# Kernel optimization log

Measured on AMD Instinct MI355X. Metric: run time of the kernel, lower is better.

## Reference

```python
import jax, jax.numpy as jnp
import numpy as np

N_NODES = 100000
N_EDGES = 3200000
NEG_SLOPE = 0.2


def setup_inputs() -> dict:
    key = jax.random.key(0)
    k = jax.random.split(key, 7)
    feat = jax.random.normal(k[0], (N_NODES, 256), dtype=jnp.float32)
    W_fc = jax.random.normal(k[1], (64, 256), dtype=jnp.float32) * 0.05
    attn_l = jax.random.normal(k[2], (4, 16), dtype=jnp.float32) * 0.1
    attn_r = jax.random.normal(k[3], (4, 16), dtype=jnp.float32) * 0.1
    W_res = jax.random.normal(k[4], (64, 256), dtype=jnp.float32) * 0.05
    src = jax.random.randint(k[5], (N_EDGES,), 0, N_NODES, dtype=jnp.int32)
    dst = jax.random.randint(k[6], (N_EDGES,), 0, N_NODES, dtype=jnp.int32)
    return {"feat": feat, "W_fc": W_fc, "attn_l": attn_l, "attn_r": attn_r,
            "W_res": W_res, "src": src, "dst": dst}


def reference(feat, W_fc, attn_l, attn_r, W_res, src, dst):
    N = feat.shape[0]
    H, D = attn_l.shape
    # Linear projection -> per-head features [N, H, D]
    feat_src = (feat @ W_fc.T).reshape(N, H, D)
    # Per-node attention logits [N, H]
    el = jnp.einsum('nhd,hd->nh', feat_src, attn_l)
    er = jnp.einsum('nhd,hd->nh', feat_src, attn_r)
    # fused_gat: per-edge leaky-relu score, edge softmax over dst, scatter-sum
    e = jax.nn.leaky_relu(el[src] + er[dst], negative_slope=NEG_SLOPE)  # [E, H]
    emax = jax.ops.segment_max(e, dst, num_segments=N)  # [N, H]
    emax = jnp.where(jnp.isfinite(emax), emax, 0.0)  # zero-degree safety
    ee = jnp.exp(e - emax[dst])  # [E, H]
    denom = jax.ops.segment_sum(ee, dst, num_segments=N)  # [N, H]
    alpha = ee / jnp.maximum(denom[dst], 1e-20)  # [E, H]
    # weighted aggregation of source features -> [N, H, D]
    rst = jax.ops.segment_sum(alpha[:, :, None] * feat_src[src], dst,
                              num_segments=N)
    # residual connection (res_fc always present in this module)
    resval = (feat @ W_res.T).reshape(N, H, D)
    return rst + resval
```

## Files before the change

### kernel.cpp

```cpp
#include <hip/hip_runtime.h>
#include <hip/hip_bf16.h>


#define F_IN 256
#define O_OUT 64
#define NEG_SLOPE 0.2f
#define CHUNK 16384
#define RMAX 2048

using frag_ab = __attribute__((ext_vector_type(8))) short;
using frag_cd = __attribute__((ext_vector_type(4))) float;

__device__ __forceinline__ float lrelu(float x) {
    return x >= 0.0f ? x : NEG_SLOPE * x;
}

__device__ __forceinline__ unsigned short f2bf(float f) {
    unsigned int u = __float_as_uint(f);
    unsigned int r = (u + 0x7fffu + ((u >> 16) & 1u)) >> 16;
    return (unsigned short)r;
}
__device__ __forceinline__ float bflo(unsigned int p) {
    return __uint_as_float(p << 16);
}
__device__ __forceinline__ float bfhi(unsigned int p) {
    return __uint_as_float(p & 0xffff0000u);
}

__global__ __launch_bounds__(256) void wprep_kernel(
    const float* __restrict__ Wfc, const float* __restrict__ Wres,
    unsigned short* __restrict__ Bf)
{
    int tid = blockIdx.x * 256 + threadIdx.x;
    int ct = tid >> 9;
    int lane = tid & 63;
    int ks = (tid >> 6) & 7;
    int col = ct * 16 + (lane & 15);
    int kbase = ks * 32 + (lane >> 4) * 8;
    const float* srcW = (col < 64) ? (Wfc + (size_t)col * 256 + kbase)
                                   : (Wres + (size_t)(col - 64) * 256 + kbase);
    unsigned short* dstp = Bf + (size_t)tid * 8;
#pragma unroll
    for (int i = 0; i < 8; ++i) dstp[i] = f2bf(srcW[i]);
}

__global__ __launch_bounds__(256) void proj_mfma_kernel(
    const float* __restrict__ feat, const unsigned short* __restrict__ Bf,
    const float* __restrict__ attn_l, const float* __restrict__ attn_r,
    unsigned short* __restrict__ fsb, float* __restrict__ el,
    float* __restrict__ er, float* __restrict__ out,
    float* __restrict__ denom_zero, int N)
{
    __shared__ __align__(16) unsigned short sA[64 * 280];
    const int t = threadIdx.x;
    const int lane = t & 63;
    const int w = t >> 6;
    const int n0 = blockIdx.x * 64;
    if (n0 >= N) return;

    frag_ab bfrag[2][8];
    {
        const unsigned short* bp = Bf + (size_t)lane * 8;
#pragma unroll
        for (int j = 0; j < 2; ++j)
#pragma unroll
            for (int ks = 0; ks < 8; ++ks)
                bfrag[j][ks] = *(const frag_ab*)(bp + (size_t)((2 * w + j) * 8 + ks) * 512);
    }

    if (denom_zero && n0 * 4 + t < N * 4) denom_zero[n0 * 4 + t] = 0.0f;

    for (int i = 0; i < 8; ++i) {
        int f = i * 256 + t;
        int row = f >> 5, c8 = f & 31;
        int n = n0 + row;
        float4 v0 = make_float4(0.f, 0.f, 0.f, 0.f), v1 = v0;
        if (n < N) {
            const float4* p = (const float4*)(feat + (size_t)n * F_IN + c8 * 8);
            v0 = p[0]; v1 = p[1];
        }
        frag_ab pack;
        pack[0] = (short)f2bf(v0.x); pack[1] = (short)f2bf(v0.y);
        pack[2] = (short)f2bf(v0.z); pack[3] = (short)f2bf(v0.w);
        pack[4] = (short)f2bf(v1.x); pack[5] = (short)f2bf(v1.y);
        pack[6] = (short)f2bf(v1.z); pack[7] = (short)f2bf(v1.w);
        *(frag_ab*)(&sA[row * 280 + c8 * 8]) = pack;
    }
    __syncthreads();

    frag_cd acc[4][2];
#pragma unroll
    for (int rt = 0; rt < 4; ++rt)
#pragma unroll
        for (int j = 0; j < 2; ++j)
            acc[rt][j] = (frag_cd){0.f, 0.f, 0.f, 0.f};

#pragma unroll
    for (int ks = 0; ks < 8; ++ks) {
        frag_ab af[4];
#pragma unroll
        for (int rt = 0; rt < 4; ++rt) {
            int row = rt * 16 + (lane & 15);
            int c8 = ks * 4 + (lane >> 4);
            af[rt] = *(const frag_ab*)(&sA[row * 280 + c8 * 8]);
        }
#pragma unroll
        for (int rt = 0; rt < 4; ++rt)
#pragma unroll
            for (int j = 0; j < 2; ++j)
                acc[rt][j] = __builtin_amdgcn_mfma_f32_16x16x32_bf16(
                    af[rt], bfrag[j][ks], acc[rt][j], 0, 0, 0);
    }

    const int colq = lane & 15;
    const int quad = lane >> 4;
    if (w < 2) {
#pragma unroll
        for (int j = 0; j < 2; ++j) {
            int h = 2 * w + j;
            float al = attn_l[h * 16 + colq];
            float ar = attn_r[h * 16 + colq];
#pragma unroll
            for (int rt = 0; rt < 4; ++rt)
#pragma unroll
                for (int r = 0; r < 4; ++r) {
                    int node = n0 + rt * 16 + quad * 4 + r;
                    float v = acc[rt][j][r];
                    if (node < N) fsb[(size_t)node * O_OUT + h * 16 + colq] = f2bf(v);
                    float pl = v * al, pr = v * ar;
                    pl += __shfl_xor(pl, 1); pr += __shfl_xor(pr, 1);
                    pl += __shfl_xor(pl, 2); pr += __shfl_xor(pr, 2);
                    pl += __shfl_xor(pl, 4); pr += __shfl_xor(pr, 4);
                    pl += __shfl_xor(pl, 8); pr += __shfl_xor(pr, 8);
                    if (colq == 0 && node < N) {
                        el[(size_t)node * 4 + h] = pl;
                        er[(size_t)node * 4 + h] = pr;
                    }
                }
        }
    } else {
#pragma unroll
        for (int j = 0; j < 2; ++j) {
            int cb = 32 * (w - 2) + 16 * j;
#pragma unroll
            for (int rt = 0; rt < 4; ++rt)
#pragma unroll
                for (int r = 0; r < 4; ++r) {
                    int node = n0 + rt * 16 + quad * 4 + r;
                    if (node < N)
                        out[(size_t)node * O_OUT + cb + colq] = acc[rt][j][r];
                }
        }
    }
}

__global__ __launch_bounds__(256) void bucket_count_kernel(
    const int* __restrict__ dst, int* __restrict__ histT, int E, int B, int R)
{
    __shared__ int h[RMAX];
    int b = blockIdx.x, t = threadIdx.x;
    for (int i = t; i < R; i += 256) h[i] = 0;
    __syncthreads();
    int base = b * CHUNK;
    for (int i = t; i < CHUNK; i += 256) {
        int e = base + i;
        if (e < E) atomicAdd(&h[dst[e] >> 7], 1);
    }
    __syncthreads();
    for (int i = t; i < R; i += 256) histT[(size_t)i * B + b] = h[i];
}

__global__ __launch_bounds__(256) void scan_block_kernel(
    const int* __restrict__ counts, int* __restrict__ outp,
    int* __restrict__ bsums, int n)
{
    int t = threadIdx.x;
    int base = blockIdx.x * 1024 + t * 4;
    int c0 = 0, c1 = 0, c2 = 0, c3 = 0;
    if (base + 3 < n) {
        int4 v = *(const int4*)(counts + base);
        c0 = v.x; c1 = v.y; c2 = v.z; c3 = v.w;
    } else {
        if (base     < n) c0 = counts[base];
        if (base + 1 < n) c1 = counts[base + 1];
        if (base + 2 < n) c2 = counts[base + 2];
        if (base + 3 < n) c3 = counts[base + 3];
    }
    int tsum = c0 + c1 + c2 + c3;
    int inc = tsum;
    int lane = t & 63, wid = t >> 6;
#pragma unroll
    for (int o = 1; o < 64; o <<= 1) {
        int v = __shfl_up(inc, o);
        if (lane >= o) inc += v;
    }
    __shared__ int wsum[4];
    if (lane == 63) wsum[wid] = inc;
    __syncthreads();
    int woff = 0;
#pragma unroll
    for (int w = 0; w < 4; ++w)
        if (w < wid) woff += wsum[w];
    int excl = woff + inc - tsum;
    int e0 = excl, e1 = excl + c0, e2 = e1 + c1, e3 = e2 + c2;
    if (base + 3 < n) {
        *(int4*)(outp + base) = make_int4(e0, e1, e2, e3);
    } else {
        if (base     < n) outp[base]     = e0;
        if (base + 1 < n) outp[base + 1] = e1;
        if (base + 2 < n) outp[base + 2] = e2;
        if (base + 3 < n) outp[base + 3] = e3;
    }
    if (t == 255) bsums[blockIdx.x] = wsum[0] + wsum[1] + wsum[2] + wsum[3];
}

__global__ void scan_bsums_kernel(int* __restrict__ bsums, int nb)
{
    int lane = threadIdx.x;
    int carry = 0;
    for (int c = 0; c * 64 < nb; ++c) {
        int i = c * 64 + lane;
        int v = (i < nb) ? bsums[i] : 0;
        int inc = v;
#pragma unroll
        for (int o = 1; o < 64; o <<= 1) {
            int u = __shfl_up(inc, o);
            if (lane >= o) inc += u;
        }
        if (i < nb) bsums[i] = carry + inc - v;
        carry += __shfl(inc, 63);
    }
}

__global__ __launch_bounds__(256) void scan_final_kernel(
    int* __restrict__ outp, const int* __restrict__ bsums, int n, int total)
{
    int i = blockIdx.x * 256 + threadIdx.x;
    if (i < n) outp[i] = outp[i] + bsums[i >> 10];
    if (i == 0) outp[n] = total;
}

__global__ __launch_bounds__(256) void bucket_scatter_kernel(
    const int* __restrict__ src, const int* __restrict__ dst,
    const int* __restrict__ histS, unsigned int* __restrict__ sorted_pk,
    int E, int B, int R)
{
    __shared__ int h[RMAX];
    __shared__ int basebin[RMAX];
    int b = blockIdx.x, t = threadIdx.x;
    for (int i = t; i < R; i += 256) {
        h[i] = 0;
        basebin[i] = histS[(size_t)i * B + b];
    }
    __syncthreads();
    int base = b * CHUNK;
    for (int i = t; i < CHUNK; i += 256) {
        int e = base + i;
        if (e < E) {
            int d = dst[e];
            int bin = d >> 7;
            int rk = atomicAdd(&h[bin], 1);
            sorted_pk[basebin[bin] + rk] =
                ((unsigned int)src[e] << 7) | (unsigned int)(d & 127);
        }
    }
}

__global__ __launch_bounds__(256) void bucket_build_kernel(
    const int* __restrict__ histS, const unsigned int* __restrict__ sorted_pk,
    int* __restrict__ rowptr, int* __restrict__ sorted_src,
    int N, int E, int B, int R)
{
    __shared__ unsigned int buf[8192];
    __shared__ int hist[128], scn[128], cur[128];
    int r = blockIdx.x, t = threadIdx.x;
    int start = histS[(size_t)r * B];
    int end = (r + 1 < R) ? histS[(size_t)(r + 1) * B] : E;
    int cnt = end - start;
    if (t < 128) hist[t] = 0;
    __syncthreads();
    bool use_lds = (cnt <= 8192);
    for (int i = t; i < cnt; i += 256) {
        unsigned int pk = sorted_pk[start + i];
        if (use_lds) buf[i] = pk;
        atomicAdd(&hist[pk & 127], 1);
    }
    __syncthreads();
    if (t < 128) scn[t] = hist[t];
    __syncthreads();
    for (int o = 1; o < 128; o <<= 1) {
        int v = 0;
        if (t < 128 && t >= o) v = scn[t - o];
        __syncthreads();
        if (t < 128) scn[t] += v;
        __syncthreads();
    }
    if (t < 128) {
        int node = r * 128 + t;
        if (node < N) rowptr[node] = start + scn[t] - hist[t];
        cur[t] = 0;
    }
    if (r == 0 && t == 0) rowptr[N] = E;
    __syncthreads();
    for (int i = t; i < cnt; i += 256) {
        unsigned int pk = use_lds ? buf[i] : sorted_pk[start + i];
        int low = pk & 127;
        int rk = atomicAdd(&cur[low], 1);
        sorted_src[start + (scn[low] - hist[low]) + rk] = (int)(pk >> 7);
    }
}

__global__ __launch_bounds__(256) void agg_csr_kernel(
    const int* __restrict__ rowptr, const int* __restrict__ srt,
    const unsigned short* __restrict__ fsb, const float* __restrict__ el,
    const float* __restrict__ er, float* __restrict__ out, int N)
{
    int d = blockIdx.x * 4 + (threadIdx.x >> 6);
    if (d >= N) return;
    const int lane = threadIdx.x & 63;
    const int half = lane >> 5;
    const int c = lane & 31;
    const int h = c >> 3;
    const int k0 = rowptr[d], k1 = rowptr[d + 1];
    const float erh = er[(size_t)d * 4 + h];
    float a0 = 0.f, a1 = 0.f, den = 0.f;

    int kb = k0;
    for (; kb + 8 <= k1; kb += 8) {
        int s0 = srt[kb + half];
        int s1 = srt[kb + 2 + half];
        int s2 = srt[kb + 4 + half];
        int s3 = srt[kb + 6 + half];
        float e0 = el[(size_t)s0 * 4 + h];
        float e1 = el[(size_t)s1 * 4 + h];
        float e2 = el[(size_t)s2 * 4 + h];
        float e3 = el[(size_t)s3 * 4 + h];
        unsigned int f0 = *(const unsigned int*)(fsb + (size_t)s0 * O_OUT + 2 * c);
        unsigned int f1 = *(const unsigned int*)(fsb + (size_t)s1 * O_OUT + 2 * c);
        unsigned int f2 = *(const unsigned int*)(fsb + (size_t)s2 * O_OUT + 2 * c);
        unsigned int f3 = *(const unsigned int*)(fsb + (size_t)s3 * O_OUT + 2 * c);
        float w0 = __expf(lrelu(e0 + erh));
        float w1 = __expf(lrelu(e1 + erh));
        float w2 = __expf(lrelu(e2 + erh));
        float w3 = __expf(lrelu(e3 + erh));
        a0 += w0 * bflo(f0); a1 += w0 * bfhi(f0); den += w0;
        a0 += w1 * bflo(f1); a1 += w1 * bfhi(f1); den += w1;
        a0 += w2 * bflo(f2); a1 += w2 * bfhi(f2); den += w2;
        a0 += w3 * bflo(f3); a1 += w3 * bfhi(f3); den += w3;
    }
    for (; kb < k1; kb += 2) {
        int ki = kb + half;
        if (ki < k1) {
            int s = srt[ki];
            float w = __expf(lrelu(el[(size_t)s * 4 + h] + erh));
            unsigned int f = *(const unsigned int*)(fsb + (size_t)s * O_OUT + 2 * c);
            a0 += w * bflo(f); a1 += w * bfhi(f); den += w;
        }
    }
    a0 += __shfl_xor(a0, 32);
    a1 += __shfl_xor(a1, 32);
    den += __shfl_xor(den, 32);
    if (half == 0) {
        float inv = 1.0f / fmaxf(den, 1e-20f);
        float2* po = (float2*)(out + (size_t)d * O_OUT + 2 * c);
        float2 o = *po;
        o.x += a0 * inv;
        o.y += a1 * inv;
        *po = o;
    }
}

__global__ __launch_bounds__(256) void edge_sum_kernel(
    const int* __restrict__ src, const int* __restrict__ dst,
    const float* __restrict__ el, const float* __restrict__ er,
    float* __restrict__ denom, int E)
{
    int e = blockIdx.x * 256 + threadIdx.x;
    if (e >= E) return;
    int s = src[e], d = dst[e];
    float4 l4 = ((const float4*)el)[s];
    float4 r4 = ((const float4*)er)[d];
    unsafeAtomicAdd(&denom[(size_t)d * 4 + 0], __expf(lrelu(l4.x + r4.x)));
    unsafeAtomicAdd(&denom[(size_t)d * 4 + 1], __expf(lrelu(l4.y + r4.y)));
    unsafeAtomicAdd(&denom[(size_t)d * 4 + 2], __expf(lrelu(l4.z + r4.z)));
    unsafeAtomicAdd(&denom[(size_t)d * 4 + 3], __expf(lrelu(l4.w + r4.w)));
}

__global__ __launch_bounds__(256) void agg_atomic_kernel(
    const int* __restrict__ src, const int* __restrict__ dst,
    const unsigned short* __restrict__ fsb, const float* __restrict__ el,
    const float* __restrict__ er, const float* __restrict__ denom,
    float* __restrict__ out, int E)
{
    const int lane = threadIdx.x & 63;
    const int wid = threadIdx.x >> 6;
    int e = blockIdx.x * 4 + wid;
    if (e >= E) return;
    int s = src[e], d = dst[e];
    int h = lane >> 4;
    float v = __expf(lrelu(el[(size_t)s * 4 + h] + er[(size_t)d * 4 + h]));
    float alpha = v / fmaxf(denom[(size_t)d * 4 + h], 1e-20f);
    float fval = __uint_as_float(((unsigned int)fsb[(size_t)s * O_OUT + lane]) << 16);
    unsafeAtomicAdd(&out[(size_t)d * O_OUT + lane], alpha * fval);
}

extern "C" void kernel_launch(void* const* d_in, const int* in_sizes, int n_in,
                              void* d_out, int out_size, void* d_ws, size_t ws_size,
                              hipStream_t stream) {
    const float* feat   = (const float*)d_in[0];
    const float* Wfc    = (const float*)d_in[1];
    const float* attn_l = (const float*)d_in[2];
    const float* attn_r = (const float*)d_in[3];
    const float* Wres   = (const float*)d_in[4];
    const int*   src    = (const int*)d_in[5];
    const int*   dst    = (const int*)d_in[6];

    const int N = in_sizes[0] / F_IN;
    const int E = in_sizes[5];
    float* out = (float*)d_out;

    const int R = (N + 127) >> 7;
    const int B = (E + CHUNK - 1) / CHUNK;
    const int nRB = R * B;

    float* el     = (float*)d_ws;
    float* er     = el + (size_t)N * 4;
    unsigned short* Bf = (unsigned short*)(er + (size_t)N * 4);
    int*   histT  = (int*)(Bf + 32768);
    int*   histS  = histT + nRB;
    int*   bsums  = histS + nRB + 8;
    int*   rowptr = bsums + 1024;
    unsigned int* sorted_pk = (unsigned int*)(rowptr + N + 4);
    int*   sorted_src = (int*)(sorted_pk + E);
    unsigned short* fsb = (unsigned short*)(sorted_src + E);
    size_t need_main = (size_t)((char*)(fsb + (size_t)N * O_OUT) - (char*)d_ws);

    int nproj = (N + 63) / 64;

    if (ws_size >= need_main && R <= RMAX) {
        wprep_kernel<<<16, 256, 0, stream>>>(Wfc, Wres, Bf);
        proj_mfma_kernel<<<nproj, 256, 0, stream>>>(
            feat, Bf, attn_l, attn_r, fsb, el, er, out, nullptr, N);
        bucket_count_kernel<<<B, 256, 0, stream>>>(dst, histT, E, B, R);
        int nsb = (nRB + 1023) / 1024;
        scan_block_kernel<<<nsb, 256, 0, stream>>>(histT, histS, bsums, nRB);
        scan_bsums_kernel<<<1, 64, 0, stream>>>(bsums, nsb);
        scan_final_kernel<<<(nRB + 255) / 256, 256, 0, stream>>>(histS, bsums, nRB, E);
        bucket_scatter_kernel<<<B, 256, 0, stream>>>(src, dst, histS, sorted_pk, E, B, R);
        bucket_build_kernel<<<R, 256, 0, stream>>>(
            histS, sorted_pk, rowptr, sorted_src, N, E, B, R);
        agg_csr_kernel<<<(N + 3) / 4, 256, 0, stream>>>(
            rowptr, sorted_src, fsb, el, er, out, N);
    } else {
        float* denom = (float*)histT;
        unsigned short* fsb2 = (unsigned short*)(denom + (size_t)N * 4);
        wprep_kernel<<<16, 256, 0, stream>>>(Wfc, Wres, Bf);
        proj_mfma_kernel<<<nproj, 256, 0, stream>>>(
            feat, Bf, attn_l, attn_r, fsb2, el, er, out, denom, N);
        edge_sum_kernel<<<(E + 255) / 256, 256, 0, stream>>>(src, dst, el, er, denom, E);
        agg_atomic_kernel<<<(E + 3) / 4, 256, 0, stream>>>(
            src, dst, fsb2, el, er, denom, out, E);
    }
}
```

Before: 455.3 us.

## Fuse CSR build and aggregation into per-bucket LDS atomic accumulation kernel

Removes the per-bucket CSR construction pass (rowptr and sorted_src) and instead aggregates directly from the bucket-sorted packed edges. One 512-thread block per 128-node bucket accumulates numerators and denominators in LDS with atomics. The fsb column layout is permuted so each lane's bf16 pair maps to fixed output channels, and CHUNK shrinks to cut scatter contention. This saves a kernel and a global write/read of sorted_src, at the cost of heavy LDS atomic traffic and lower parallelism (about 782 blocks).

After: 1.723 ms. +278.4%, slower.

```diff
diff --git a/kernel.cpp b/kernel.cpp
--- a/kernel.cpp
+++ b/kernel.cpp
@@ -5,7 +5,7 @@
 #define F_IN 256
 #define O_OUT 64
 #define NEG_SLOPE 0.2f
-#define CHUNK 16384
+#define CHUNK 4096
 #define RMAX 2048
 
 using frag_ab = __attribute__((ext_vector_type(8))) short;
@@ -25,6 +25,16 @@
 }
 __device__ __forceinline__ float bfhi(unsigned int p) {
     return __uint_as_float(p & 0xffff0000u);
+}
+
+__device__ __forceinline__ int fsb_pos(int ch) {
+    int h = ch >> 4;
+    int jp = ch & 15;
+    int hi2 = h >> 1;
+    int jj = jp & 7;
+    int c_lane = 8 * h + jj;
+    int is_ch0 = (hi2 == 0) ? (jp < 8) : (jp >= 8);
+    return 2 * c_lane + (is_ch0 ? 0 : 1);
 }
 
 __global__ __launch_bounds__(256) void wprep_kernel(
@@ -120,13 +130,14 @@
             int h = 2 * w + j;
             float al = attn_l[h * 16 + colq];
             float ar = attn_r[h * 16 + colq];
+            int pos = fsb_pos(h * 16 + colq);
 #pragma unroll
             for (int rt = 0; rt < 4; ++rt)
 #pragma unroll
                 for (int r = 0; r < 4; ++r) {
                     int node = n0 + rt * 16 + quad * 4 + r;
                     float v = acc[rt][j][r];
-                    if (node < N) fsb[(size_t)node * O_OUT + h * 16 + colq] = f2bf(v);
+                    if (node < N) fsb[(size_t)node * O_OUT + pos] = f2bf(v);
                     float pl = v * al, pr = v * ar;
                     pl += __shfl_xor(pl, 1); pr += __shfl_xor(pr, 1);
                     pl += __shfl_xor(pl, 2); pr += __shfl_xor(pr, 2);
@@ -266,107 +277,89 @@
     }
 }
 
-__global__ __launch_bounds__(256) void bucket_build_kernel(
+__global__ __launch_bounds__(512) void agg_fused_kernel(
     const int* __restrict__ histS, const unsigned int* __restrict__ sorted_pk,
-    int* __restrict__ rowptr, int* __restrict__ sorted_src,
+    const unsigned short* __restrict__ fsb, const float* __restrict__ el,
+    const float* __restrict__ er, float* __restrict__ out,
     int N, int E, int B, int R)
 {
-    __shared__ unsigned int buf[8192];
-    __shared__ int hist[128], scn[128], cur[128];
-    int r = blockIdx.x, t = threadIdx.x;
-    int start = histS[(size_t)r * B];
-    int end = (r + 1 < R) ? histS[(size_t)(r + 1) * B] : E;
-    int cnt = end - start;
-    if (t < 128) hist[t] = 0;
-    __syncthreads();
-    bool use_lds = (cnt <= 8192);
-    for (int i = t; i < cnt; i += 256) {
-        unsigned int pk = sorted_pk[start + i];
-        if (use_lds) buf[i] = pk;
-        atomicAdd(&hist[pk & 127], 1);
-    }
-    __syncthreads();
-    if (t < 128) scn[t] = hist[t];
-    __syncthreads();
-    for (int o = 1; o < 128; o <<= 1) {
-        int v = 0;
-        if (t < 128 && t >= o) v = scn[t - o];
-        __syncthreads();
-        if (t < 128) scn[t] += v;
-        __syncthreads();
-    }
-    if (t < 128) {
-        int node = r * 128 + t;
-        if (node < N) rowptr[node] = start + scn[t] - hist[t];
-        cur[t] = 0;
-    }
-    if (r == 0 && t == 0) rowptr[N] = E;
-    __syncthreads();
-    for (int i = t; i < cnt; i += 256) {
-        unsigned int pk = use_lds ? buf[i] : sorted_pk[start + i];
-        int low = pk & 127;
-        int rk = atomicAdd(&cur[low], 1);
-        sorted_src[start + (scn[low] - hist[low]) + rk] = (int)(pk >> 7);
-    }
-}
-
-__global__ __launch_bounds__(256) void agg_csr_kernel(
-    const int* __restrict__ rowptr, const int* __restrict__ srt,
-    const unsigned short* __restrict__ fsb, const float* __restrict__ el,
-    const float* __restrict__ er, float* __restrict__ out, int N)
-{
-    int d = blockIdx.x * 4 + (threadIdx.x >> 6);
-    if (d >= N) return;
-    const int lane = threadIdx.x & 63;
+    __shared__ float num[128][64];
+    __shared__ float den[128][4];
+    __shared__ float er_s[512];
+    const int r = blockIdx.x;
+    const int t = threadIdx.x;
+
+    float* np = &num[0][0];
+    for (int i = t; i < 128 * 64; i += 512) np[i] = 0.f;
+    ((float*)den)[t] = 0.f;
+    int gn = r * 512 + t;
+    er_s[t] = (gn < N * 4) ? er[gn] : 0.f;
+    __syncthreads();
+
+    const int start = histS[(size_t)r * B];
+    const int end = (r + 1 < R) ? histS[(size_t)(r + 1) * B] : E;
+    const int lane = t & 63;
+    const int wid = t >> 6;
     const int half = lane >> 5;
     const int c = lane & 31;
     const int h = c >> 3;
-    const int k0 = rowptr[d], k1 = rowptr[d + 1];
-    const float erh = er[(size_t)d * 4 + h];
-    float a0 = 0.f, a1 = 0.f, den = 0.f;
-
-    int kb = k0;
-    for (; kb + 8 <= k1; kb += 8) {
-        int s0 = srt[kb + half];
-        int s1 = srt[kb + 2 + half];
-        int s2 = srt[kb + 4 + half];
-        int s3 = srt[kb + 6 + half];
-        float e0 = el[(size_t)s0 * 4 + h];
-        float e1 = el[(size_t)s1 * 4 + h];
-        float e2 = el[(size_t)s2 * 4 + h];
-        float e3 = el[(size_t)s3 * 4 + h];
-        unsigned int f0 = *(const unsigned int*)(fsb + (size_t)s0 * O_OUT + 2 * c);
-        unsigned int f1 = *(const unsigned int*)(fsb + (size_t)s1 * O_OUT + 2 * c);
-        unsigned int f2 = *(const unsigned int*)(fsb + (size_t)s2 * O_OUT + 2 * c);
-        unsigned int f3 = *(const unsigned int*)(fsb + (size_t)s3 * O_OUT + 2 * c);
-        float w0 = __expf(lrelu(e0 + erh));
-        float w1 = __expf(lrelu(e1 + erh));
-        float w2 = __expf(lrelu(e2 + erh));
-        float w3 = __expf(lrelu(e3 + erh));
-        a0 += w0 * bflo(f0); a1 += w0 * bfhi(f0); den += w0;
-        a0 += w1 * bflo(f1); a1 += w1 * bfhi(f1); den += w1;
-        a0 += w2 * bflo(f2); a1 += w2 * bfhi(f2); den += w2;
-        a0 += w3 * bflo(f3); a1 += w3 * bfhi(f3); den += w3;
-    }
-    for (; kb < k1; kb += 2) {
-        int ki = kb + half;
-        if (ki < k1) {
-            int s = srt[ki];
-            float w = __expf(lrelu(el[(size_t)s * 4 + h] + erh));
-            unsigned int f = *(const unsigned int*)(fsb + (size_t)s * O_OUT + 2 * c);
-            a0 += w * bflo(f); a1 += w * bfhi(f); den += w;
-        }
-    }
-    a0 += __shfl_xor(a0, 32);
-    a1 += __shfl_xor(a1, 32);
-    den += __shfl_xor(den, 32);
-    if (half == 0) {
-        float inv = 1.0f / fmaxf(den, 1e-20f);
-        float2* po = (float2*)(out + (size_t)d * O_OUT + 2 * c);
-        float2 o = *po;
-        o.x += a0 * inv;
-        o.y += a1 * inv;
-        *po = o;
+    const int hi2 = h >> 1;
+    const int ch0 = 16 * h + (c & 7) + 8 * hi2;
+    const int ch1 = 16 * h + (c & 7) + 8 * (1 - hi2);
+
+    int kb = start + wid * 16;
+    for (; kb + 16 <= end; kb += 8 * 16) {
+        unsigned int pk[8];
+#pragma unroll
+        for (int p = 0; p < 8; ++p) pk[p] = sorted_pk[kb + 2 * p + half];
+        float elv[8]; unsigned int fv[8]; int dl[8];
+#pragma unroll
+        for (int p = 0; p < 8; ++p) {
+            int s = (int)(pk[p] >> 7);
+            dl[p] = (int)(pk[p] & 127u);
+            elv[p] = el[(size_t)s * 4 + h];
+            fv[p] = *(const unsigned int*)(fsb + (size_t)s * O_OUT + 2 * c);
+        }
+#pragma unroll
+        for (int p = 0; p < 8; ++p) {
+            float wv = __expf(lrelu(elv[p] + er_s[dl[p] * 4 + h]));
+            atomicAdd(&num[dl[p]][ch0], wv * bflo(fv[p]));
+            atomicAdd(&num[dl[p]][ch1], wv * bfhi(fv[p]));
+            if ((c & 7) == 0) atomicAdd(&den[dl[p]][h], wv);
+        }
+    }
+    {
+        int tb = start + ((end - start) & ~15);
+        if (wid == 0) {
+            for (int kb2 = tb + half; kb2 < end; kb2 += 2) {
+                unsigned int pk = sorted_pk[kb2];
+                int s = (int)(pk >> 7);
+                int dl2 = (int)(pk & 127u);
+                float wv = __expf(lrelu(el[(size_t)s * 4 + h] + er_s[dl2 * 4 + h]));
+                unsigned int f = *(const unsigned int*)(fsb + (size_t)s * O_OUT + 2 * c);
+                atomicAdd(&num[dl2][ch0], wv * bflo(f));
+                atomicAdd(&num[dl2][ch1], wv * bfhi(f));
+                if ((c & 7) == 0) atomicAdd(&den[dl2][h], wv);
+            }
+        }
+    }
+    __syncthreads();
+
+#pragma unroll
+    for (int i = 0; i < 4; ++i) {
+        int idx = i * 2048 + t * 4;
+        int row = idx >> 6;
+        int ch = idx & 63;
+        int node = r * 128 + row;
+        if (node < N) {
+            float inv = 1.0f / fmaxf(den[row][ch >> 4], 1e-20f);
+            float4 v = *(const float4*)(&num[row][ch]);
+            float4* po = (float4*)(out + (size_t)node * O_OUT + ch);
+            float4 o = *po;
+            o.x += v.x * inv; o.y += v.y * inv;
+            o.z += v.z * inv; o.w += v.w * inv;
+            *po = o;
+        }
     }
 }
 
@@ -398,10 +391,14 @@
     if (e >= E) return;
     int s = src[e], d = dst[e];
     int h = lane >> 4;
+    int jj = (lane >> 1) & 7;
+    int hi2 = (lane >> 5) & 1;
+    int odd = lane & 1;
+    int ch = 16 * h + jj + 8 * (hi2 ^ odd);
     float v = __expf(lrelu(el[(size_t)s * 4 + h] + er[(size_t)d * 4 + h]));
     float alpha = v / fmaxf(denom[(size_t)d * 4 + h], 1e-20f);
     float fval = __uint_as_float(((unsigned int)fsb[(size_t)s * O_OUT + lane]) << 16);
-    unsafeAtomicAdd(&out[(size_t)d * O_OUT + lane], alpha * fval);
+    unsafeAtomicAdd(&out[(size_t)d * O_OUT + ch], alpha * fval);
 }
 
 extern "C" void kernel_launch(void* const* d_in, const int* in_sizes, int n_in,
@@ -422,6 +419,7 @@
     const int R = (N + 127) >> 7;
     const int B = (E + CHUNK - 1) / CHUNK;
     const int nRB = R * B;
+    const int nsb = (nRB + 1023) / 1024;
 
     float* el     = (float*)d_ws;
     float* er     = el + (size_t)N * 4;
@@ -429,28 +427,23 @@
     int*   histT  = (int*)(Bf + 32768);
     int*   histS  = histT + nRB;
     int*   bsums  = histS + nRB + 8;
-    int*   rowptr = bsums + 1024;
-    unsigned int* sorted_pk = (unsigned int*)(rowptr + N + 4);
-    int*   sorted_src = (int*)(sorted_pk + E);
-    unsigned short* fsb = (unsigned short*)(sorted_src + E);
+    unsigned int* sorted_pk = (unsigned int*)(bsums + 1024);
+    unsigned short* fsb = (unsigned short*)(sorted_pk + E);
     size_t need_main = (size_t)((char*)(fsb + (size_t)N * O_OUT) - (char*)d_ws);
 
     int nproj = (N + 63) / 64;
 
-    if (ws_size >= need_main && R <= RMAX) {
+    if (ws_size >= need_main && R <= RMAX && nsb <= 1024) {
         wprep_kernel<<<16, 256, 0, stream>>>(Wfc, Wres, Bf);
         proj_mfma_kernel<<<nproj, 256, 0, stream>>>(
             feat, Bf, attn_l, attn_r, fsb, el, er, out, nullptr, N);
         bucket_count_kernel<<<B, 256, 0, stream>>>(dst, histT, E, B, R);
-        int nsb = (nRB + 1023) / 1024;
         scan_block_kernel<<<nsb, 256, 0, stream>>>(histT, histS, bsums, nRB);
         scan_bsums_kernel<<<1, 64, 0, stream>>>(bsums, nsb);
         scan_final_kernel<<<(nRB + 255) / 256, 256, 0, stream>>>(histS, bsums, nRB, E);
         bucket_scatter_kernel<<<B, 256, 0, stream>>>(src, dst, histS, sorted_pk, E, B, R);
-        bucket_build_kernel<<<R, 256, 0, stream>>>(
-            histS, sorted_pk, rowptr, sorted_src, N, E, B, R);
-        agg_csr_kernel<<<(N + 3) / 4, 256, 0, stream>>>(
-            rowptr, sorted_src, fsb, el, er, out, N);
+        agg_fused_kernel<<<R, 512, 0, stream>>>(
+            histS, sorted_pk, fsb, el, er, out, N, E, B, R);
     } else {
         float* denom = (float*)histT;
         unsigned short* fsb2 = (unsigned short*)(denom + (size_t)N * 4);
```

## Replace two-level bucket sort CSR build with global atomic counting sort

Applied to the files above, without the earlier changes.

Replaces the LDS-based two-pass bucket sort (per-chunk bucket histograms, scatter into buckets, then per-bucket local sort) with a simple per-node counting sort. Per-destination counts come from global atomics, are prefix-scanned into rowptr, and a scatter pass uses atomicSub to place each source. This removes the intermediate packed array and the bucket-build pass, at the cost of heavy global atomic traffic on random addresses and a nondeterministic edge order within each row.

New measurement: 597.4 us. 31.2% more time.

```diff
diff --git a/kernel.cpp b/kernel.cpp
--- a/kernel.cpp
+++ b/kernel.cpp
@@ -5,8 +5,6 @@
 #define F_IN 256
 #define O_OUT 64
 #define NEG_SLOPE 0.2f
-#define CHUNK 16384
-#define RMAX 2048
 
 using frag_ab = __attribute__((ext_vector_type(8))) short;
 using frag_cd = __attribute__((ext_vector_type(4))) float;
@@ -154,20 +152,29 @@
     }
 }
 
-__global__ __launch_bounds__(256) void bucket_count_kernel(
-    const int* __restrict__ dst, int* __restrict__ histT, int E, int B, int R)
-{
-    __shared__ int h[RMAX];
-    int b = blockIdx.x, t = threadIdx.x;
-    for (int i = t; i < R; i += 256) h[i] = 0;
-    __syncthreads();
-    int base = b * CHUNK;
-    for (int i = t; i < CHUNK; i += 256) {
-        int e = base + i;
-        if (e < E) atomicAdd(&h[dst[e] >> 7], 1);
-    }
-    __syncthreads();
-    for (int i = t; i < R; i += 256) histT[(size_t)i * B + b] = h[i];
+__global__ __launch_bounds__(256) void zero_kernel(int* __restrict__ p, int n)
+{
+    int i = blockIdx.x * 256 + threadIdx.x;
+    if (i < n) p[i] = 0;
+}
+
+__global__ __launch_bounds__(256) void hist_kernel(
+    const int* __restrict__ dst, int* __restrict__ count, int E)
+{
+    int e = blockIdx.x * 256 + threadIdx.x;
+    if (e < E) atomicAdd(&count[dst[e]], 1);
+}
+
+__global__ __launch_bounds__(256) void scatter_csr_kernel(
+    const int* __restrict__ src, const int* __restrict__ dst,
+    const int* __restrict__ rowptr, int* __restrict__ count,
+    int* __restrict__ sorted_src, int E)
+{
+    int e = blockIdx.x * 256 + threadIdx.x;
+    if (e >= E) return;
+    int d = dst[e];
+    int old = atomicSub(&count[d], 1);
+    sorted_src[rowptr[d] + old - 1] = src[e];
 }
 
 __global__ __launch_bounds__(256) void scan_block_kernel(
@@ -238,76 +245,6 @@
     int i = blockIdx.x * 256 + threadIdx.x;
     if (i < n) outp[i] = outp[i] + bsums[i >> 10];
     if (i == 0) outp[n] = total;
-}
-
-__global__ __launch_bounds__(256) void bucket_scatter_kernel(
-    const int* __restrict__ src, const int* __restrict__ dst,
-    const int* __restrict__ histS, unsigned int* __restrict__ sorted_pk,
-    int E, int B, int R)
-{
-    __shared__ int h[RMAX];
-    __shared__ int basebin[RMAX];
-    int b = blockIdx.x, t = threadIdx.x;
-    for (int i = t; i < R; i += 256) {
-        h[i] = 0;
-        basebin[i] = histS[(size_t)i * B + b];
-    }
-    __syncthreads();
-    int base = b * CHUNK;
-    for (int i = t; i < CHUNK; i += 256) {
-        int e = base + i;
-        if (e < E) {
-            int d = dst[e];
-            int bin = d >> 7;
-            int rk = atomicAdd(&h[bin], 1);
-            sorted_pk[basebin[bin] + rk] =
-                ((unsigned int)src[e] << 7) | (unsigned int)(d & 127);
-        }
-    }
-}
-
-__global__ __launch_bounds__(256) void bucket_build_kernel(
-    const int* __restrict__ histS, const unsigned int* __restrict__ sorted_pk,
-    int* __restrict__ rowptr, int* __restrict__ sorted_src,
-    int N, int E, int B, int R)
-{
-    __shared__ unsigned int buf[8192];
-    __shared__ int hist[128], scn[128], cur[128];
-    int r = blockIdx.x, t = threadIdx.x;
-    int start = histS[(size_t)r * B];
-    int end = (r + 1 < R) ? histS[(size_t)(r + 1) * B] : E;
-    int cnt = end - start;
-    if (t < 128) hist[t] = 0;
-    __syncthreads();
-    bool use_lds = (cnt <= 8192);
-    for (int i = t; i < cnt; i += 256) {
-        unsigned int pk = sorted_pk[start + i];
-        if (use_lds) buf[i] = pk;
-        atomicAdd(&hist[pk & 127], 1);
-    }
-    __syncthreads();
-    if (t < 128) scn[t] = hist[t];
-    __syncthreads();
-    for (int o = 1; o < 128; o <<= 1) {
-        int v = 0;
-        if (t < 128 && t >= o) v = scn[t - o];
-        __syncthreads();
-        if (t < 128) scn[t] += v;
-        __syncthreads();
-    }
-    if (t < 128) {
-        int node = r * 128 + t;
-        if (node < N) rowptr[node] = start + scn[t] - hist[t];
-        cur[t] = 0;
-    }
-    if (r == 0 && t == 0) rowptr[N] = E;
-    __syncthreads();
-    for (int i = t; i < cnt; i += 256) {
-        unsigned int pk = use_lds ? buf[i] : sorted_pk[start + i];
-        int low = pk & 127;
-        int rk = atomicAdd(&cur[low], 1);
-        sorted_src[start + (scn[low] - hist[low]) + rk] = (int)(pk >> 7);
-    }
 }
 
 __global__ __launch_bounds__(256) void agg_csr_kernel(
@@ -419,40 +356,34 @@
     const int E = in_sizes[5];
     float* out = (float*)d_out;
 
-    const int R = (N + 127) >> 7;
-    const int B = (E + CHUNK - 1) / CHUNK;
-    const int nRB = R * B;
-
     float* el     = (float*)d_ws;
     float* er     = el + (size_t)N * 4;
     unsigned short* Bf = (unsigned short*)(er + (size_t)N * 4);
-    int*   histT  = (int*)(Bf + 32768);
-    int*   histS  = histT + nRB;
-    int*   bsums  = histS + nRB + 8;
-    int*   rowptr = bsums + 1024;
-    unsigned int* sorted_pk = (unsigned int*)(rowptr + N + 4);
-    int*   sorted_src = (int*)(sorted_pk + E);
+    int*   count  = (int*)(Bf + 32768);
+    int*   rowptr = count + N;
+    int*   bsums  = rowptr + N + 4;
+    int*   sorted_src = bsums + 1024;
     unsigned short* fsb = (unsigned short*)(sorted_src + E);
     size_t need_main = (size_t)((char*)(fsb + (size_t)N * O_OUT) - (char*)d_ws);
 
     int nproj = (N + 63) / 64;
-
-    if (ws_size >= need_main && R <= RMAX) {
+    int nsb = (N + 1023) / 1024;
+
+    if (ws_size >= need_main && nsb <= 1024) {
         wprep_kernel<<<16, 256, 0, stream>>>(Wfc, Wres, Bf);
         proj_mfma_kernel<<<nproj, 256, 0, stream>>>(
             feat, Bf, attn_l, attn_r, fsb, el, er, out, nullptr, N);
-        bucket_count_kernel<<<B, 256, 0, stream>>>(dst, histT, E, B, R);
-        int nsb = (nRB + 1023) / 1024;
-        scan_block_kernel<<<nsb, 256, 0, stream>>>(histT, histS, bsums, nRB);
+        zero_kernel<<<(N + 255) / 256, 256, 0, stream>>>(count, N);
+        hist_kernel<<<(E + 255) / 256, 256, 0, stream>>>(dst, count, E);
+        scan_block_kernel<<<nsb, 256, 0, stream>>>(count, rowptr, bsums, N);
         scan_bsums_kernel<<<1, 64, 0, stream>>>(bsums, nsb);
-        scan_final_kernel<<<(nRB + 255) / 256, 256, 0, stream>>>(histS, bsums, nRB, E);
-        bucket_scatter_kernel<<<B, 256, 0, stream>>>(src, dst, histS, sorted_pk, E, B, R);
-        bucket_build_kernel<<<R, 256, 0, stream>>>(
-            histS, sorted_pk, rowptr, sorted_src, N, E, B, R);
+        scan_final_kernel<<<(N + 255) / 256, 256, 0, stream>>>(rowptr, bsums, N, E);
+        scatter_csr_kernel<<<(E + 255) / 256, 256, 0, stream>>>(
+            src, dst, rowptr, count, sorted_src, E);
         agg_csr_kernel<<<(N + 3) / 4, 256, 0, stream>>>(
             rowptr, sorted_src, fsb, el, er, out, N);
     } else {
-        float* denom = (float*)histT;
+        float* denom = (float*)count;
         unsigned short* fsb2 = (unsigned short*)(denom + (size_t)N * 4);
         wprep_kernel<<<16, 256, 0, stream>>>(Wfc, Wres, Bf);
         proj_mfma_kernel<<<nproj, 256, 0, stream>>>(
```

## Fuse CSR bucket build with aggregation in a single per-bucket kernel

Applied to the files above, without the earlier changes.

Replaces the separate bucket build kernel and per-node CSR aggregation kernel with one kernel per 128-node bucket. It sorts the bucket's source indices into LDS and then aggregates its nodes directly. This removes the global sorted_src and rowptr writes and reads and one kernel launch. The trade-off is a much smaller grid with each wave processing 16 nodes serially, which may reduce latency hiding for the gathers. There is also a slow fallback scan for oversized buckets.

Result: no change. 455.6 us (+0.1%).

```diff
diff --git a/kernel.cpp b/kernel.cpp
--- a/kernel.cpp
+++ b/kernel.cpp
@@ -266,25 +266,27 @@
     }
 }
 
-__global__ __launch_bounds__(256) void bucket_build_kernel(
+__global__ __launch_bounds__(512) void agg_bucket_kernel(
     const int* __restrict__ histS, const unsigned int* __restrict__ sorted_pk,
-    int* __restrict__ rowptr, int* __restrict__ sorted_src,
+    const unsigned short* __restrict__ fsb, const float* __restrict__ el,
+    const float* __restrict__ er, float* __restrict__ out,
     int N, int E, int B, int R)
 {
-    __shared__ unsigned int buf[8192];
+    __shared__ int buf2[8192];
     __shared__ int hist[128], scn[128], cur[128];
-    int r = blockIdx.x, t = threadIdx.x;
+    const int r = blockIdx.x;
+    const int t = threadIdx.x;
     int start = histS[(size_t)r * B];
     int end = (r + 1 < R) ? histS[(size_t)(r + 1) * B] : E;
-    int cnt = end - start;
-    if (t < 128) hist[t] = 0;
-    __syncthreads();
-    bool use_lds = (cnt <= 8192);
-    for (int i = t; i < cnt; i += 256) {
-        unsigned int pk = sorted_pk[start + i];
-        if (use_lds) buf[i] = pk;
-        atomicAdd(&hist[pk & 127], 1);
-    }
+    if (start < 0) start = 0;
+    if (end < start) end = start;
+    if (end > E) end = E;
+    const int cnt = end - start;
+
+    if (t < 128) { hist[t] = 0; cur[t] = 0; }
+    __syncthreads();
+    for (int i = t; i < cnt; i += 512)
+        atomicAdd(&hist[sorted_pk[start + i] & 127], 1);
     __syncthreads();
     if (t < 128) scn[t] = hist[t];
     __syncthreads();
@@ -295,78 +297,88 @@
         if (t < 128) scn[t] += v;
         __syncthreads();
     }
-    if (t < 128) {
-        int node = r * 128 + t;
-        if (node < N) rowptr[node] = start + scn[t] - hist[t];
-        cur[t] = 0;
-    }
-    if (r == 0 && t == 0) rowptr[N] = E;
-    __syncthreads();
-    for (int i = t; i < cnt; i += 256) {
-        unsigned int pk = use_lds ? buf[i] : sorted_pk[start + i];
-        int low = pk & 127;
-        int rk = atomicAdd(&cur[low], 1);
-        sorted_src[start + (scn[low] - hist[low]) + rk] = (int)(pk >> 7);
-    }
-}
-
-__global__ __launch_bounds__(256) void agg_csr_kernel(
-    const int* __restrict__ rowptr, const int* __restrict__ srt,
-    const unsigned short* __restrict__ fsb, const float* __restrict__ el,
-    const float* __restrict__ er, float* __restrict__ out, int N)
-{
-    int d = blockIdx.x * 4 + (threadIdx.x >> 6);
-    if (d >= N) return;
-    const int lane = threadIdx.x & 63;
+    const bool use_lds = (cnt <= 8192);
+    if (use_lds) {
+        for (int i = t; i < cnt; i += 512) {
+            unsigned int pk = sorted_pk[start + i];
+            int low = (int)(pk & 127u);
+            int rk = atomicAdd(&cur[low], 1);
+            buf2[(scn[low] - hist[low]) + rk] = (int)(pk >> 7);
+        }
+    }
+    __syncthreads();
+
+    const int lane = t & 63;
+    const int w = t >> 6;
     const int half = lane >> 5;
     const int c = lane & 31;
     const int h = c >> 3;
-    const int k0 = rowptr[d], k1 = rowptr[d + 1];
-    const float erh = er[(size_t)d * 4 + h];
-    float a0 = 0.f, a1 = 0.f, den = 0.f;
-
-    int kb = k0;
-    for (; kb + 8 <= k1; kb += 8) {
-        int s0 = srt[kb + half];
-        int s1 = srt[kb + 2 + half];
-        int s2 = srt[kb + 4 + half];
-        int s3 = srt[kb + 6 + half];
-        float e0 = el[(size_t)s0 * 4 + h];
-        float e1 = el[(size_t)s1 * 4 + h];
-        float e2 = el[(size_t)s2 * 4 + h];
-        float e3 = el[(size_t)s3 * 4 + h];
-        unsigned int f0 = *(const unsigned int*)(fsb + (size_t)s0 * O_OUT + 2 * c);
-        unsigned int f1 = *(const unsigned int*)(fsb + (size_t)s1 * O_OUT + 2 * c);
-        unsigned int f2 = *(const unsigned int*)(fsb + (size_t)s2 * O_OUT + 2 * c);
-        unsigned int f3 = *(const unsigned int*)(fsb + (size_t)s3 * O_OUT + 2 * c);
-        float w0 = __expf(lrelu(e0 + erh));
-        float w1 = __expf(lrelu(e1 + erh));
-        float w2 = __expf(lrelu(e2 + erh));
-        float w3 = __expf(lrelu(e3 + erh));
-        a0 += w0 * bflo(f0); a1 += w0 * bfhi(f0); den += w0;
-        a0 += w1 * bflo(f1); a1 += w1 * bfhi(f1); den += w1;
-        a0 += w2 * bflo(f2); a1 += w2 * bfhi(f2); den += w2;
-        a0 += w3 * bflo(f3); a1 += w3 * bfhi(f3); den += w3;
-    }
-    for (; kb < k1; kb += 2) {
-        int ki = kb + half;
-        if (ki < k1) {
-            int s = srt[ki];
-            float w = __expf(lrelu(el[(size_t)s * 4 + h] + erh));
-            unsigned int f = *(const unsigned int*)(fsb + (size_t)s * O_OUT + 2 * c);
-            a0 += w * bflo(f); a1 += w * bfhi(f); den += w;
-        }
-    }
-    a0 += __shfl_xor(a0, 32);
-    a1 += __shfl_xor(a1, 32);
-    den += __shfl_xor(den, 32);
-    if (half == 0) {
-        float inv = 1.0f / fmaxf(den, 1e-20f);
-        float2* po = (float2*)(out + (size_t)d * O_OUT + 2 * c);
-        float2 o = *po;
-        o.x += a0 * inv;
-        o.y += a1 * inv;
-        *po = o;
+    for (int j = 0; j < 16; ++j) {
+        int dl = w * 16 + j;
+        int d = r * 128 + dl;
+        if (d >= N) break;
+        const int k0 = scn[dl] - hist[dl];
+        const int k1 = scn[dl];
+        const float erh = er[(size_t)d * 4 + h];
+        float a0 = 0.f, a1 = 0.f, den = 0.f;
+        if (use_lds) {
+            int kb = k0;
+            for (; kb + 8 <= k1; kb += 8) {
+                int s0 = buf2[kb + half];
+                int s1 = buf2[kb + 2 + half];
+                int s2 = buf2[kb + 4 + half];
+                int s3 = buf2[kb + 6 + half];
+                float e0 = el[(size_t)s0 * 4 + h];
+                float e1 = el[(size_t)s1 * 4 + h];
+                float e2 = el[(size_t)s2 * 4 + h];
+                float e3 = el[(size_t)s3 * 4 + h];
+                unsigned int f0 = *(const unsigned int*)(fsb + (size_t)s0 * O_OUT + 2 * c);
+                unsigned int f1 = *(const unsigned int*)(fsb + (size_t)s1 * O_OUT + 2 * c);
+                unsigned int f2 = *(const unsigned int*)(fsb + (size_t)s2 * O_OUT + 2 * c);
+                unsigned int f3 = *(const unsigned int*)(fsb + (size_t)s3 * O_OUT + 2 * c);
+                float w0 = __expf(lrelu(e0 + erh));
+                float w1 = __expf(lrelu(e1 + erh));
+                float w2 = __expf(lrelu(e2 + erh));
+                float w3 = __expf(lrelu(e3 + erh));
+                a0 += w0 * bflo(f0); a1 += w0 * bfhi(f0); den += w0;
+                a0 += w1 * bflo(f1); a1 += w1 * bfhi(f1); den += w1;
+                a0 += w2 * bflo(f2); a1 += w2 * bfhi(f2); den += w2;
+                a0 += w3 * bflo(f3); a1 += w3 * bfhi(f3); den += w3;
+            }
+            for (; kb < k1; kb += 2) {
+                int ki = kb + half;
+                if (ki < k1) {
+                    int s = buf2[ki];
+                    float wv = __expf(lrelu(el[(size_t)s * 4 + h] + erh));
+                    unsigned int f = *(const unsigned int*)(fsb + (size_t)s * O_OUT + 2 * c);
+                    a0 += wv * bflo(f); a1 += wv * bfhi(f); den += wv;
+                }
+            }
+        } else {
+            for (int i2 = 0; i2 < cnt; i2 += 2) {
+                int ki = i2 + half;
+                if (ki < cnt) {
+                    unsigned int pk = sorted_pk[start + ki];
+                    if ((int)(pk & 127u) == dl) {
+                        int s = (int)(pk >> 7);
+                        float wv = __expf(lrelu(el[(size_t)s * 4 + h] + erh));
+                        unsigned int f = *(const unsigned int*)(fsb + (size_t)s * O_OUT + 2 * c);
+                        a0 += wv * bflo(f); a1 += wv * bfhi(f); den += wv;
+                    }
+                }
+            }
+        }
+        a0 += __shfl_xor(a0, 32);
+        a1 += __shfl_xor(a1, 32);
+        den += __shfl_xor(den, 32);
+        if (half == 0) {
+            float inv = 1.0f / fmaxf(den, 1e-20f);
+            float2* po = (float2*)(out + (size_t)d * O_OUT + 2 * c);
+            float2 o = *po;
+            o.x += a0 * inv;
+            o.y += a1 * inv;
+            *po = o;
+        }
     }
 }
 
@@ -422,6 +434,7 @@
     const int R = (N + 127) >> 7;
     const int B = (E + CHUNK - 1) / CHUNK;
     const int nRB = R * B;
+    const int nsb = (nRB + 1023) / 1024;
 
     float* el     = (float*)d_ws;
     float* er     = el + (size_t)N * 4;
@@ -429,28 +442,23 @@
     int*   histT  = (int*)(Bf + 32768);
     int*   histS  = histT + nRB;
     int*   bsums  = histS + nRB + 8;
-    int*   rowptr = bsums + 1024;
-    unsigned int* sorted_pk = (unsigned int*)(rowptr + N + 4);
-    int*   sorted_src = (int*)(sorted_pk + E);
-    unsigned short* fsb = (unsigned short*)(sorted_src + E);
+    unsigned int* sorted_pk = (unsigned int*)(bsums + 1024);
+    unsigned short* fsb = (unsigned short*)(sorted_pk + E);
     size_t need_main = (size_t)((char*)(fsb + (size_t)N * O_OUT) - (char*)d_ws);
 
     int nproj = (N + 63) / 64;
 
-    if (ws_size >= need_main && R <= RMAX) {
+    if (ws_size >= need_main && R <= RMAX && nsb <= 1024) {
         wprep_kernel<<<16, 256, 0, stream>>>(Wfc, Wres, Bf);
         proj_mfma_kernel<<<nproj, 256, 0, stream>>>(
             feat, Bf, attn_l, attn_r, fsb, el, er, out, nullptr, N);
         bucket_count_kernel<<<B, 256, 0, stream>>>(dst, histT, E, B, R);
-        int nsb = (nRB + 1023) / 1024;
         scan_block_kernel<<<nsb, 256, 0, stream>>>(histT, histS, bsums, nRB);
         scan_bsums_kernel<<<1, 64, 0, stream>>>(bsums, nsb);
         scan_final_kernel<<<(nRB + 255) / 256, 256, 0, stream>>>(histS, bsums, nRB, E);
         bucket_scatter_kernel<<<B, 256, 0, stream>>>(src, dst, histS, sorted_pk, E, B, R);
-        bucket_build_kernel<<<R, 256, 0, stream>>>(
-            histS, sorted_pk, rowptr, sorted_src, N, E, B, R);
-        agg_csr_kernel<<<(N + 3) / 4, 256, 0, stream>>>(
-            rowptr, sorted_src, fsb, el, er, out, N);
+        agg_bucket_kernel<<<R, 512, 0, stream>>>(
+            histS, sorted_pk, fsb, el, er, out, N, E, B, R);
     } else {
         float* denom = (float*)histT;
         unsigned short* fsb2 = (unsigned short*)(denom + (size_t)N * 4);
```
